# Kernel optimization log

Measured on AMD Instinct MI355X. Metric: run time of the kernel, lower is better.

Reference implementation:

```python
import jax, jax.numpy as jnp
import numpy as np

NEG = -1e9


def setup_inputs() -> dict:
    key = jax.random.key(0)
    k1, k2, k3, k4 = jax.random.split(key, 4)
    R, N, D = 64, 200000, 256
    hs = jax.random.normal(k1, (R, D), dtype=jnp.float32)
    es = jax.random.normal(k2, (N, D), dtype=jnp.float32)
    W = jax.random.normal(k3, (D, D), dtype=jnp.float32) / np.sqrt(D)
    mask = jax.random.randint(k4, (R, N), 0, 2) > 0
    return {"hs": hs, "es": es, "W": W, "mask": mask, "n_output": 50}


def reference(hs, es, W, mask, n_output):
    # MatchingLayer: bilinear match scores[r, n] = hs_r^T W es_n  -> [R, N]
    original_scores = (hs @ W) @ es.T
    mu = original_scores.mean()
    std = original_scores.std(ddof=1)  # torch .std() is unbiased
    scores = (original_scores - mu) / std
    # logits used for expansion scores (differentiable)
    logits = jax.nn.log_softmax(scores, axis=-1) + jax.nn.log_softmax(scores, axis=0)
    # detached probabilities for selection
    d = jax.lax.stop_gradient(scores)
    row_probs = jnp.maximum(jax.nn.softmax(jnp.where(mask, d, NEG), axis=-1), 1e-6)
    col_probs = jnp.maximum(jax.nn.softmax(jnp.where(mask, d, NEG), axis=0), 1e-6)
    # deterministic (eval) path: assign each candidate to its argmax category
    index = jnp.argmax(col_probs, axis=0)  # [N]
    R = scores.shape[0]
    valid = mask & (index[None, :] == jnp.arange(R)[:, None])  # [R, N]
    sel = jnp.where(valid, row_probs, -jnp.inf)
    top_vals, top_idx = jax.lax.top_k(sel, n_output)  # [R, n_output]
    ok = jnp.isfinite(top_vals)  # rows with fewer candidates than n_output -> padded
    expansions = jnp.where(ok, top_idx, -1)  # [R, n_output], -1 = pad
    # expansion_scores[i] = logits[:, expansion_i].T -> [n_output, R]
    exp_scores = jnp.transpose(logits[:, top_idx], (1, 2, 0))  # [R, n_output, R]
    exp_scores = exp_scores * ok[:, :, None].astype(exp_scores.dtype)
    return expansions, exp_scores
```

## Files before the change

kernel.cpp:

```cpp
#include <hip/hip_runtime.h>
#include <math.h>

#define RR 64
#define DD 256
#define CAP 6144


__device__ __forceinline__ void get_mu_istd(const double* sums, int N, float& fmu, float& istd) {
  double M = (double)RR * (double)N;
  double mu = sums[0] / M;
  double var = (sums[1] - sums[0] * sums[0] / M) / (M - 1.0);
  fmu = (float)mu;
  istd = (float)(1.0 / sqrt(var));
}


__global__ __launch_bounds__(256) void k_mask(const void* __restrict__ maskp,
                                              unsigned long long* __restrict__ mbits,
                                              int N) {
  __shared__ int f;
  int tid = threadIdx.x;
  if (tid == 0) f = 0;
  __syncthreads();
  {
    const unsigned* mw = (const unsigned*)maskp;
    int mode = 0;
    for (int i = tid; i < 4096; i += 256) {
      unsigned v = mw[i];
      if (v == 0x3f800000u) mode = 2;
      else if (v > 1u && mode != 2) mode = 1;
    }
    if (mode) atomicMax(&f, mode);
  }
  __syncthreads();
  const int mode = f;

  int n = blockIdx.x * 256 + tid;
  if (n >= N) return;
  unsigned long long b = 0;
  if (mode == 1) {
    const unsigned char* m = (const unsigned char*)maskp;
#pragma unroll
    for (int r = 0; r < RR; ++r)
      b |= (unsigned long long)(m[(size_t)r * N + n] != 0) << r;
  } else if (mode == 2) {
    const float* m = (const float*)maskp;
#pragma unroll
    for (int r = 0; r < RR; ++r)
      b |= (unsigned long long)(m[(size_t)r * N + n] != 0.f) << r;
  } else {
    const int* m = (const int*)maskp;
#pragma unroll
    for (int r = 0; r < RR; ++r)
      b |= (unsigned long long)(m[(size_t)r * N + n] != 0) << r;
  }
  mbits[n] = b;
}


__global__ __launch_bounds__(256) void k_hsw(const float* __restrict__ hs,
                                             const float* __restrict__ W,
                                             float* __restrict__ hsW) {
  int i = blockIdx.x;
  int j = threadIdx.x;
  float acc = 0.f;
  for (int k = 0; k < DD; ++k) acc = fmaf(hs[i * DD + k], W[k * DD + j], acc);
  hsW[i * DD + j] = acc;
}


__global__ __launch_bounds__(256) void k_scores(const float* __restrict__ es,
                                                const float* __restrict__ hsW,
                                                const unsigned long long* __restrict__ mbits,
                                                float* __restrict__ scores,
                                                float* __restrict__ colmax,
                                                int* __restrict__ colargmax,
                                                float* __restrict__ qpart,
                                                double* __restrict__ spart,
                                                int N) {
  __shared__ float lds[256 * 36];
  __shared__ float wlds[64 * 32];
  __shared__ double red[8];
  const int tid = threadIdx.x;
  const int lane = tid & 63;
  const int ty = __builtin_amdgcn_readfirstlane(tid >> 6);
  const int n0 = blockIdx.x * 256;
  const int R0 = ty * 16;
  const int nb = n0 + lane;

  const int ec = tid >> 3;
  const int ek = (tid & 7) * 4;
  const int wrow = tid >> 2;
  const int wk = (tid & 3) * 8;

  float4 acc[16];
#pragma unroll
  for (int i = 0; i < 16; ++i) acc[i] = make_float4(0.f, 0.f, 0.f, 0.f);

  float4 er[8], wr0, wr1;
#pragma unroll
  for (int p = 0; p < 8; ++p) {
    int c = p * 32 + ec;
    int rr = min(n0 + c, N - 1);
    er[p] = *(const float4*)(es + (size_t)rr * DD + ek);
  }
  wr0 = *(const float4*)(hsW + wrow * DD + wk);
  wr1 = *(const float4*)(hsW + wrow * DD + wk + 4);

  for (int kc = 0; kc < DD; kc += 32) {
    __syncthreads();
#pragma unroll
    for (int p = 0; p < 8; ++p) {
      int c = p * 32 + ec;
      *(float4*)(lds + c * 36 + ek) = er[p];
    }
    *(float4*)(wlds + wrow * 32 + wk) = wr0;
    *(float4*)(wlds + wrow * 32 + wk + 4) = wr1;
    if (kc + 32 < DD) {
#pragma unroll
      for (int p = 0; p < 8; ++p) {
        int c = p * 32 + ec;
        int rr = min(n0 + c, N - 1);
        er[p] = *(const float4*)(es + (size_t)rr * DD + kc + 32 + ek);
      }
      wr0 = *(const float4*)(hsW + wrow * DD + kc + 32 + wk);
      wr1 = *(const float4*)(hsW + wrow * DD + kc + 32 + wk + 4);
    }
    __syncthreads();
#pragma unroll
    for (int k = 0; k < 32; k += 4) {
      const float4 e0 = *(const float4*)(lds + (lane +   0) * 36 + k);
      const float4 e1 = *(const float4*)(lds + (lane +  64) * 36 + k);
      const float4 e2 = *(const float4*)(lds + (lane + 128) * 36 + k);
      const float4 e3 = *(const float4*)(lds + (lane + 192) * 36 + k);
#pragma unroll
      for (int i = 0; i < 16; ++i) {
        const float4 w = *(const float4*)(wlds + (R0 + i) * 32 + k);
        acc[i].x = fmaf(w.x, e0.x, fmaf(w.y, e0.y, fmaf(w.z, e0.z, fmaf(w.w, e0.w, acc[i].x))));
        acc[i].y = fmaf(w.x, e1.x, fmaf(w.y, e1.y, fmaf(w.z, e1.z, fmaf(w.w, e1.w, acc[i].y))));
        acc[i].z = fmaf(w.x, e2.x, fmaf(w.y, e2.y, fmaf(w.z, e2.z, fmaf(w.w, e2.w, acc[i].z))));
        acc[i].w = fmaf(w.x, e3.x, fmaf(w.y, e3.y, fmaf(w.z, e3.z, fmaf(w.w, e3.w, acc[i].w))));
      }
    }
  }

  bool val[4];
#pragma unroll
  for (int c = 0; c < 4; ++c) val[c] = (nb + 64 * c) < N;

#pragma unroll
  for (int i = 0; i < 16; ++i) {
    float* dst = scores + (size_t)(R0 + i) * N + nb;
    float v[4] = {acc[i].x, acc[i].y, acc[i].z, acc[i].w};
#pragma unroll
    for (int c = 0; c < 4; ++c)
      if (val[c]) dst[64 * c] = v[c];
  }

  unsigned long long mb[4];
#pragma unroll
  for (int c = 0; c < 4; ++c) mb[c] = val[c] ? mbits[nb + 64 * c] : 0ull;

  float ps1[4], ps2[4], pcm[4], pbv[4];
  int pbr[4];
#pragma unroll
  for (int c = 0; c < 4; ++c) { ps1[c] = 0.f; ps2[c] = 0.f; pcm[c] = -INFINITY; pbv[c] = -INFINITY; pbr[c] = -1; }

#pragma unroll
  for (int i = 0; i < 16; ++i) {
    const int rrow = R0 + i;
    float v[4] = {acc[i].x, acc[i].y, acc[i].z, acc[i].w};
    float q = -INFINITY, qm = -INFINITY;
#pragma unroll
    for (int c = 0; c < 4; ++c) {
      ps1[c] += v[c];
      ps2[c] = fmaf(v[c], v[c], ps2[c]);
      pcm[c] = fmaxf(pcm[c], v[c]);
      bool bit = (mb[c] >> rrow) & 1ull;
      if (bit && (v[c] > pbv[c])) { pbv[c] = v[c]; pbr[c] = rrow; }
      float qv = val[c] ? v[c] : -INFINITY;
      q = fmaxf(q, qv);
      if (bit) qm = fmaxf(qm, qv);
    }
#pragma unroll
    for (int o = 32; o > 0; o >>= 1) {
      q = fmaxf(q, __shfl_down(q, o));
      qm = fmaxf(qm, __shfl_down(qm, o));
    }
    if (lane == 0) {
      qpart[(size_t)blockIdx.x * 128 + rrow] = q;
      qpart[(size_t)blockIdx.x * 128 + 64 + rrow] = qm;
    }
  }

  __syncthreads();
  float* Ls1 = lds;
  float* Ls2 = lds + 1024;
  float* Lcm = lds + 2048;
  float* Lbv = lds + 3072;
  int* Lbr = (int*)(lds + 4096);
#pragma unroll
  for (int c = 0; c < 4; ++c) {
    int col = lane + 64 * c;
    Ls1[ty * 256 + col] = ps1[c];
    Ls2[ty * 256 + col] = ps2[c];
    Lcm[ty * 256 + col] = pcm[c];
    Lbv[ty * 256 + col] = pbv[c];
    Lbr[ty * 256 + col] = pbr[c];
  }
  __syncthreads();

  const int n = n0 + tid;
  float s1 = 0.f, s2 = 0.f;
  if (n < N) {
    s1 = Ls1[tid] + Ls1[256 + tid] + Ls1[512 + tid] + Ls1[768 + tid];
    s2 = Ls2[tid] + Ls2[256 + tid] + Ls2[512 + tid] + Ls2[768 + tid];
    float cm = fmaxf(fmaxf(Lcm[tid], Lcm[256 + tid]), fmaxf(Lcm[512 + tid], Lcm[768 + tid]));
    colmax[n] = cm;
    float bv = -INFINITY;
    int br = -1;
#pragma unroll
    for (int w2 = 0; w2 < 4; ++w2) {
      float b = Lbv[w2 * 256 + tid];
      if (b > bv) { bv = b; br = Lbr[w2 * 256 + tid]; }
    }
    colargmax[n] = br;
  }

  double d1 = (double)s1, d2 = (double)s2;
#pragma unroll
  for (int o = 32; o > 0; o >>= 1) {
    d1 += __shfl_down(d1, o);
    d2 += __shfl_down(d2, o);
  }
  if ((tid & 63) == 0) { red[ty * 2] = d1; red[ty * 2 + 1] = d2; }
  __syncthreads();
  if (tid == 0) {
    spart[(size_t)blockIdx.x * 2] = red[0] + red[2] + red[4] + red[6];
    spart[(size_t)blockIdx.x * 2 + 1] = red[1] + red[3] + red[5] + red[7];
  }
}


__global__ __launch_bounds__(256) void k_redmax(const float* __restrict__ qpart,
                                                float* __restrict__ rowmaxf,
                                                int NBlk) {
  const int slot = blockIdx.x;
  const int tid = threadIdx.x, lane = tid & 63, ty = tid >> 6;
  __shared__ float w[4];
  float m = -INFINITY;
  for (int i = tid; i < NBlk; i += 256) m = fmaxf(m, qpart[(size_t)i * 128 + slot]);
#pragma unroll
  for (int o = 32; o > 0; o >>= 1) m = fmaxf(m, __shfl_down(m, o));
  if (lane == 0) w[ty] = m;
  __syncthreads();
  if (tid == 0) rowmaxf[slot] = fmaxf(fmaxf(w[0], w[1]), fmaxf(w[2], w[3]));
}


__global__ __launch_bounds__(256) void k_redsum(const double* __restrict__ spart,
                                                double* __restrict__ sums,
                                                int NBlk) {
  const int tid = threadIdx.x, lane = tid & 63, ty = tid >> 6;
  __shared__ double r[8];
  double s0 = 0.0, s1 = 0.0;
  for (int i = tid; i < NBlk; i += 256) {
    s0 += spart[(size_t)i * 2];
    s1 += spart[(size_t)i * 2 + 1];
  }
#pragma unroll
  for (int o = 32; o > 0; o >>= 1) {
    s0 += __shfl_down(s0, o);
    s1 += __shfl_down(s1, o);
  }
  if (lane == 0) { r[ty * 2] = s0; r[ty * 2 + 1] = s1; }
  __syncthreads();
  if (tid == 0) {
    sums[0] = r[0] + r[2] + r[4] + r[6];
    sums[1] = r[1] + r[3] + r[5] + r[7];
  }
}


__global__ __launch_bounds__(256) void k_colpass(const float* __restrict__ scores,
                                                 const float* __restrict__ colmax,
                                                 const int* __restrict__ colargmax,
                                                 const unsigned long long* __restrict__ mbits,
                                                 const double* __restrict__ sums,
                                                 const float* __restrict__ rowmaxf,
                                                 float* __restrict__ collse,
                                                 float* __restrict__ colpart,
                                                 int* __restrict__ cnt,
                                                 float* __restrict__ candx,
                                                 int* __restrict__ candn,
                                                 int N) {
  __shared__ float rmS[64], suS[64], smS[64];
  __shared__ float rpu[64 * 4], rpm[64 * 4];
  __shared__ int lcnt[64], lbase[64];
  const int tid = threadIdx.x, lane = tid & 63, ty = tid >> 6;
  float fmu, istd;
  get_mu_istd(sums, N, fmu, istd);
  if (tid < 64) {
    rmS[tid] = rowmaxf[tid];
    lcnt[tid] = 0;
  }
  __syncthreads();
  float gm = rmS[0];
#pragma unroll
  for (int r = 1; r < RR; ++r) gm = fmaxf(gm, rmS[r]);
  if (tid < 64) {
    suS[tid] = expf((gm - rmS[tid]) * istd);
    smS[tid] = expf((gm - rowmaxf[64 + tid]) * istd);
  }

  const int n = blockIdx.x * 256 + tid;
  const bool valid = n < N;
  const float cm = valid ? colmax[n] : 0.f;
  const int br = valid ? colargmax[n] : -1;
  const unsigned long long mbn = valid ? mbits[n] : 0ull;
  float colsum = 0.f, xbr = 0.f;

  for (int r = 0; r < RR; ++r) {
    float x = valid ? scores[(size_t)r * N + n] : 0.f;
    if (r == br) xbr = x;
    float E = valid ? expf((x - gm) * istd) : 0.f;
    colsum += E;
    float eu = E;
    float em = ((mbn >> r) & 1ull) ? E : 0.f;
#pragma unroll
    for (int o = 32; o > 0; o >>= 1) {
      eu += __shfl_down(eu, o);
      em += __shfl_down(em, o);
    }
    if (lane == 0) { rpu[r * 4 + ty] = eu; rpm[r * 4 + ty] = em; }
  }

  if (valid) collse[n] = logf(colsum) + (gm - cm) * istd;
  int lpos = 0;
  if (br >= 0) lpos = atomicAdd(&lcnt[br], 1);
  __syncthreads();
  if (tid < 64) {
    float su = (rpu[tid * 4] + rpu[tid * 4 + 1] + rpu[tid * 4 + 2] + rpu[tid * 4 + 3]) * suS[tid];
    float sm = (rpm[tid * 4] + rpm[tid * 4 + 1] + rpm[tid * 4 + 2] + rpm[tid * 4 + 3]) * smS[tid];
    colpart[(size_t)blockIdx.x * 128 + tid] = su;
    colpart[(size_t)blockIdx.x * 128 + 64 + tid] = sm;
    int c = lcnt[tid];
    lbase[tid] = c ? atomicAdd(&cnt[tid], c) : 0;
  }
  __syncthreads();
  if (br >= 0) {
    int pos = lbase[br] + lpos;
    if (pos < CAP) {
      candx[(size_t)br * CAP + pos] = xbr;
      candn[(size_t)br * CAP + pos] = n;
    }
  }
}


__global__ __launch_bounds__(256) void k_redacc(const float* __restrict__ colpart,
                                                const float* __restrict__ rowmaxf,
                                                float* __restrict__ rowstats,
                                                int NBlk) {
  const int slot = blockIdx.x;
  const int tid = threadIdx.x, lane = tid & 63, ty = tid >> 6;
  __shared__ float w[4];
  float s = 0.f;
  for (int i = tid; i < NBlk; i += 256) s += colpart[(size_t)i * 128 + slot];
#pragma unroll
  for (int o = 32; o > 0; o >>= 1) s += __shfl_down(s, o);
  if (lane == 0) w[ty] = s;
  __syncthreads();
  if (tid == 0) {
    float total = w[0] + w[1] + w[2] + w[3];
    if (slot < 64) {
      rowstats[slot] = rowmaxf[slot];
      rowstats[64 + slot] = logf(total);
    } else {
      rowstats[128 + (slot - 64)] = rowmaxf[slot];
      rowstats[192 + (slot - 64)] = total;
    }
  }
}


__global__ __launch_bounds__(512) void k_topk(const int* __restrict__ cnt,
                                              const float* __restrict__ candx,
                                              const int* __restrict__ candn,
                                              const double* __restrict__ sums,
                                              const float* __restrict__ rowstats,
                                              float* __restrict__ out,
                                              int* __restrict__ seln,
                                              int N, int NO) {
  int r = blockIdx.x, tid = threadIdx.x;
  __shared__ float sp[CAP];
  __shared__ int sn[CAP];
  __shared__ float wp[8];
  __shared__ int wn[8], wi[8];
  int c = min(cnt[r], CAP);
  float fmu, istd;
  get_mu_istd(sums, N, fmu, istd);
  const float rmm = rowstats[128 + r];
  const float lm = rowstats[192 + r];
  for (int i = tid; i < c; i += 512) {
    float xv = candx[(size_t)r * CAP + i];
    sp[i] = fmaxf(expf((xv - rmm) * istd) / lm, 1e-6f);
    sn[i] = candn[(size_t)r * CAP + i];
  }
  __syncthreads();
  for (int j = 0; j < NO; ++j) {
    float bp = -1.f;
    int bn = 0x7fffffff, bi = -1;
    for (int i = tid; i < c; i += 512) {
      float p = sp[i];
      int nn = sn[i];
      if (p > bp || (p == bp && nn < bn)) { bp = p; bn = nn; bi = i; }
    }
#pragma unroll
    for (int o = 32; o > 0; o >>= 1) {
      float p2 = __shfl_down(bp, o);
      int n2 = __shfl_down(bn, o);
      int i2 = __shfl_down(bi, o);
      if (p2 > bp || (p2 == bp && n2 < bn)) { bp = p2; bn = n2; bi = i2; }
    }
    if ((tid & 63) == 0) { wp[tid >> 6] = bp; wn[tid >> 6] = bn; wi[tid >> 6] = bi; }
    __syncthreads();
    if (tid == 0) {
      float fp2 = wp[0]; int fn2 = wn[0], fi2 = wi[0];
#pragma unroll
      for (int w2 = 1; w2 < 8; ++w2) {
        if (wp[w2] > fp2 || (wp[w2] == fp2 && wn[w2] < fn2)) { fp2 = wp[w2]; fn2 = wn[w2]; fi2 = wi[w2]; }
      }
      if (fp2 > 0.f) {
        out[r * NO + j] = (float)fn2;
        seln[r * NO + j] = fn2;
        sp[fi2] = -1.f;
      } else {
        out[r * NO + j] = -1.f;
        seln[r * NO + j] = -1;
      }
    }
    __syncthreads();
  }
}


__global__ void k_expand(const float* __restrict__ scores,
                         const double* __restrict__ sums,
                         const float* __restrict__ rowstats,
                         const float* __restrict__ colmax,
                         const float* __restrict__ collse,
                         const int* __restrict__ seln,
                         float* __restrict__ out,
                         int N, int NO) {
  int b = blockIdx.x;
  int r2 = threadIdx.x;
  int n = seln[b];
  float v = 0.f;
  if (n >= 0) {
    float fmu, istd;
    get_mu_istd(sums, N, fmu, istd);
    float x = scores[(size_t)r2 * N + n];
    float v1 = (x - rowstats[r2]) * istd - rowstats[64 + r2];
    float v2 = (x - colmax[n]) * istd - collse[n];
    v = v1 + v2;
  }
  out[RR * NO + (size_t)b * RR + r2] = v;
}


extern "C" void kernel_launch(void* const* d_in, const int* in_sizes, int n_in,
                              void* d_out, int out_size, void* d_ws, size_t ws_size,
                              hipStream_t stream) {
  const float* hs = (const float*)d_in[0];
  const float* es = (const float*)d_in[1];
  const float* W = (const float*)d_in[2];
  const void* mask = d_in[3];

  const int N = in_sizes[1] / DD;
  const int NO = out_size / (RR * (1 + RR));
  const int NB = (N + 255) / 256;

  char* ws = (char*)d_ws;
  size_t o = 0;
  float* scores = (float*)(ws + o);   o += (size_t)RR * N * 4;
  float* hsW = (float*)(ws + o);      o += RR * DD * 4;
  o = (o + 255) & ~(size_t)255;
  double* sums = (double*)(ws + o);
  int* cnt = (int*)(ws + o + 16);
  size_t zero_off = o, zero_bytes = 16 + 256;
  o += 512;
  float* rowstats = (float*)(ws + o); o += 256 * 4;
  float* rowmaxf = (float*)(ws + o);  o += 128 * 4;
  o = (o + 255) & ~(size_t)255;
  float* colmax = (float*)(ws + o);   o += (size_t)N * 4;
  int* colargmax = (int*)(ws + o);    o += (size_t)N * 4;
  float* collse = (float*)(ws + o);   o += (size_t)N * 4;
  o = (o + 255) & ~(size_t)255;
  unsigned long long* mbits = (unsigned long long*)(ws + o); o += (size_t)N * 8;
  o = (o + 255) & ~(size_t)255;
  float* candx = (float*)(ws + o);    o += (size_t)RR * CAP * 4;
  int* candn = (int*)(ws + o);        o += (size_t)RR * CAP * 4;
  int* seln = (int*)(ws + o);         o += (size_t)RR * NO * 4;
  o = (o + 255) & ~(size_t)255;
  float* qpart = (float*)(ws + o);    o += (size_t)NB * 128 * 4;
  double* spart = (double*)(ws + o);  o += (size_t)NB * 2 * 8;
  float* colpart = (float*)(ws + o);  o += (size_t)NB * 128 * 4;

  hipMemsetAsync(ws + zero_off, 0, zero_bytes, stream);

  k_mask<<<NB, 256, 0, stream>>>(mask, mbits, N);
  k_hsw<<<RR, 256, 0, stream>>>(hs, W, hsW);
  k_scores<<<NB, 256, 0, stream>>>(es, hsW, mbits, scores, colmax, colargmax,
                                   qpart, spart, N);
  k_redmax<<<128, 256, 0, stream>>>(qpart, rowmaxf, NB);
  k_redsum<<<1, 256, 0, stream>>>(spart, sums, NB);
  k_colpass<<<NB, 256, 0, stream>>>(scores, colmax, colargmax, mbits, sums, rowmaxf,
                                    collse, colpart, cnt, candx, candn, N);
  k_redacc<<<128, 256, 0, stream>>>(colpart, rowmaxf, rowstats, NB);
  k_topk<<<RR, 512, 0, stream>>>(cnt, candx, candn, sums, rowstats, (float*)d_out, seln,
                                 N, NO);
  k_expand<<<RR * NO, 64, 0, stream>>>(scores, sums, rowstats, colmax, collse, seln,
                                       (float*)d_out, N, NO);
}
```

Measured before the change: 659.5 us.

## Stream es/hsW tiles into LDS via direct global-to-LDS loads with double buffering

The scores GEMM kernel now loads the es and hsW tiles with direct global-to-LDS loads (global_load_lds) into two LDS buffers, instead of staging them through registers. Each tile is fetched one iteration ahead and waited on with vmcnt plus a barrier. The padded es layout is replaced by an XOR-swizzled layout to avoid bank conflicts. This is meant to cut register pressure and the VGPR-to-LDS store instructions and to overlap loads with FMA work, at the price of more LDS (80KB), which may lower occupancy.

```diff
diff --git a/kernel.cpp b/kernel.cpp
--- a/kernel.cpp
+++ b/kernel.cpp
@@ -12,6 +12,11 @@
   double var = (sums[1] - sums[0] * sums[0] / M) / (M - 1.0);
   fmu = (float)mu;
   istd = (float)(1.0 / sqrt(var));
+}
+
+__device__ __forceinline__ void cp16(const void* g, void* l) {
+  __builtin_amdgcn_global_load_lds((const __attribute__((address_space(1))) void*)g,
+                                   (__attribute__((address_space(3))) void*)l, 16, 0, 0);
 }
 
 
@@ -78,9 +83,7 @@
                                                 float* __restrict__ qpart,
                                                 double* __restrict__ spart,
                                                 int N) {
-  __shared__ float lds[256 * 36];
-  __shared__ float wlds[64 * 32];
-  __shared__ double red[8];
+  __shared__ float lds[20480];
   const int tid = threadIdx.x;
   const int lane = tid & 63;
   const int ty = __builtin_amdgcn_readfirstlane(tid >> 6);
@@ -88,60 +91,60 @@
   const int R0 = ty * 16;
   const int nb = n0 + lane;
 
-  const int ec = tid >> 3;
-  const int ek = (tid & 7) * 4;
-  const int wrow = tid >> 2;
-  const int wk = (tid & 3) * 8;
+  const int srow = ty * 8 + (lane >> 3);
+  const int sg4 = (((lane & 7) ^ ((lane >> 3) & 7)) << 2);
+  const int wrow = ty * 16 + (lane >> 2);
+  const int wg4 = (lane & 3) << 2;
 
   float4 acc[16];
 #pragma unroll
   for (int i = 0; i < 16; ++i) acc[i] = make_float4(0.f, 0.f, 0.f, 0.f);
 
-  float4 er[8], wr0, wr1;
-#pragma unroll
-  for (int p = 0; p < 8; ++p) {
-    int c = p * 32 + ec;
-    int rr = min(n0 + c, N - 1);
-    er[p] = *(const float4*)(es + (size_t)rr * DD + ek);
-  }
-  wr0 = *(const float4*)(hsW + wrow * DD + wk);
-  wr1 = *(const float4*)(hsW + wrow * DD + wk + 4);
+  auto stage = [&](float* ebase, float* wbase, int kc) {
+#pragma unroll
+    for (int p = 0; p < 8; ++p) {
+      const int col = p * 32 + srow;
+      const int rr = min(n0 + col, N - 1);
+      cp16(es + (size_t)rr * DD + kc + sg4, ebase + p * 1024 + ty * 256);
+    }
+    cp16(hsW + (size_t)wrow * DD + kc + wg4, wbase + ty * 256);
+    cp16(hsW + (size_t)wrow * DD + kc + 16 + wg4, wbase + 1024 + ty * 256);
+  };
+
+  stage(lds, lds + 16384, 0);
+  asm volatile("s_waitcnt vmcnt(0)" ::: "memory");
+  __syncthreads();
+
+  const int swz = (lane & 7);
 
   for (int kc = 0; kc < DD; kc += 32) {
-    __syncthreads();
-#pragma unroll
-    for (int p = 0; p < 8; ++p) {
-      int c = p * 32 + ec;
-      *(float4*)(lds + c * 36 + ek) = er[p];
-    }
-    *(float4*)(wlds + wrow * 32 + wk) = wr0;
-    *(float4*)(wlds + wrow * 32 + wk + 4) = wr1;
+    const int cur = (kc >> 5) & 1;
+    float* ebC = lds + (cur ? 8192 : 0);
+    float* wbC = lds + 16384 + (cur ? 2048 : 0);
     if (kc + 32 < DD) {
-#pragma unroll
-      for (int p = 0; p < 8; ++p) {
-        int c = p * 32 + ec;
-        int rr = min(n0 + c, N - 1);
-        er[p] = *(const float4*)(es + (size_t)rr * DD + kc + 32 + ek);
-      }
-      wr0 = *(const float4*)(hsW + wrow * DD + kc + 32 + wk);
-      wr1 = *(const float4*)(hsW + wrow * DD + kc + 32 + wk + 4);
-    }
-    __syncthreads();
+      float* ebN = lds + (cur ? 0 : 8192);
+      float* wbN = lds + 16384 + (cur ? 0 : 2048);
+      stage(ebN, wbN, kc + 32);
+    }
 #pragma unroll
     for (int k = 0; k < 32; k += 4) {
-      const float4 e0 = *(const float4*)(lds + (lane +   0) * 36 + k);
-      const float4 e1 = *(const float4*)(lds + (lane +  64) * 36 + k);
-      const float4 e2 = *(const float4*)(lds + (lane + 128) * 36 + k);
-      const float4 e3 = *(const float4*)(lds + (lane + 192) * 36 + k);
+      const int eswz = (((k >> 2) ^ swz) << 2);
+      const float4 e0 = *(const float4*)(ebC + (lane       ) * 32 + eswz);
+      const float4 e1 = *(const float4*)(ebC + (lane +  64 ) * 32 + eswz);
+      const float4 e2 = *(const float4*)(ebC + (lane + 128 ) * 32 + eswz);
+      const float4 e3 = *(const float4*)(ebC + (lane + 192 ) * 32 + eswz);
+      const float* wk = wbC + ((k >> 4) * 1024) + (k & 15);
 #pragma unroll
       for (int i = 0; i < 16; ++i) {
-        const float4 w = *(const float4*)(wlds + (R0 + i) * 32 + k);
+        const float4 w = *(const float4*)(wk + (R0 + i) * 16);
         acc[i].x = fmaf(w.x, e0.x, fmaf(w.y, e0.y, fmaf(w.z, e0.z, fmaf(w.w, e0.w, acc[i].x))));
         acc[i].y = fmaf(w.x, e1.x, fmaf(w.y, e1.y, fmaf(w.z, e1.z, fmaf(w.w, e1.w, acc[i].y))));
         acc[i].z = fmaf(w.x, e2.x, fmaf(w.y, e2.y, fmaf(w.z, e2.z, fmaf(w.w, e2.w, acc[i].z))));
         acc[i].w = fmaf(w.x, e3.x, fmaf(w.y, e3.y, fmaf(w.z, e3.z, fmaf(w.w, e3.w, acc[i].w))));
       }
     }
+    asm volatile("s_waitcnt vmcnt(0)" ::: "memory");
+    __syncthreads();
   }
 
   bool val[4];
@@ -199,6 +202,7 @@
   float* Lcm = lds + 2048;
   float* Lbv = lds + 3072;
   int* Lbr = (int*)(lds + 4096);
+  double* red = (double*)(lds + 5120);
 #pragma unroll
   for (int c = 0; c < 4; ++c) {
     int col = lane + 64 * c;
```

After: 632.7 us. 1.04x faster.
